# Kernel optimization log

Measured on AMD Instinct MI355X. Metric: run time of the kernel, lower is better.

## Reference

```python
import jax, jax.numpy as jnp
import numpy as np

R_MAX = 6.0
P = 6.0  # polynomial cutoff order


def poly_cutoff(r, r_max=R_MAX, p=P):
    # nequip PolynomialCutoff: smooth envelope, zero beyond r_max
    x = r / r_max
    out = (1.0
           - ((p + 1.0) * (p + 2.0) / 2.0) * x ** p
           + p * (p + 2.0) * x ** (p + 1.0)
           - (p * (p + 1.0) / 2.0) * x ** (p + 2.0))
    return out * (x < 1.0)


def setup_inputs() -> dict:
    key = jax.random.key(0)
    k1, k2, k3, k4 = jax.random.split(key, 4)
    N = 500000   # atoms
    E = 16000000  # edges
    T = 5        # species types
    edge_length = 0.5 + jax.random.uniform(k1, (E,), dtype=jnp.float32) * 5.5  # (0.5, 6.0)
    edge_index = jax.random.randint(k2, (2, E), 0, N, dtype=jnp.int64)
    species = jax.random.randint(k3, (N, 1), 0, T, dtype=jnp.int64)
    per_atom_energy = jax.random.normal(k4, (N, 1), dtype=jnp.float32)
    per_edge_scales = jnp.ones((T, T), dtype=jnp.float32)
    return {
        "edge_length": edge_length,
        "edge_index": edge_index,
        "species": species,
        "per_atom_energy": per_atom_energy,
        "per_edge_scales": per_edge_scales,
    }


def reference(edge_length, edge_index, species, per_atom_energy, per_edge_scales):
    N = species.shape[0]
    edge_center = edge_index[0]
    edge_neighbor = edge_index[1]
    sp = species[:, 0]                      # [N]
    center_sp = sp[edge_center]             # [E] gather
    neighbor_sp = sp[edge_neighbor]         # [E] gather
    l0 = per_edge_scales[center_sp, neighbor_sp]  # [E]
    # power-law repulsion with smooth cutoff
    edge_eng = (edge_length / l0) ** (-12.0) / 24.0 * l0 * poly_cutoff(edge_length)
    atom_eng = jax.ops.segment_sum(edge_eng, edge_center, num_segments=N)  # [N]
    return per_atom_energy + atom_eng[:, None]
```

## Files before the change

### kernel.cpp

```cpp
#include <hip/hip_runtime.h>
#include <stdint.h>

#define TPB_S  512
#define EPT    8
#define EPB    (TPB_S*EPT)
#define ABITS  10
#define APB    (1<<ABITS)
#define MAXB   512
#define NSH    8
#define TPB_A  1024
#define TPB_P  512
#define EDROP  1e-5f

__device__ __forceinline__ float fast_rcp(float r) {
#if defined(__has_builtin)
#if __has_builtin(__builtin_amdgcn_rcpf)
    float t = __builtin_amdgcn_rcpf(r);
    return t * fmaf(-r, t, 2.0f);
#else
    return 1.0f / r;
#endif
#else
    return 1.0f / r;
#endif
}

__device__ __forceinline__ float edge_energy_k(float r, float K) {
    float x = r * (1.0f / 6.0f);
    if (x >= 1.0f) return 0.0f;
    float x2 = x * x, x3 = x2 * x, x6 = x3 * x3;
    float cut = fmaf(x6, fmaf(x, fmaf(x, -21.0f, 48.0f), -28.0f), 1.0f);
    float t  = fast_rcp(r);
    float t2 = t * t, t4 = t2 * t2;
    float t12 = t4 * t4 * t4;
    return K * t12 * cut;
}
__device__ __forceinline__ float k_of_l0(float l0) {
    float l2 = l0 * l0, l4 = l2 * l2, l8 = l4 * l4;
    return l8 * l4 * l0 * (1.0f / 24.0f);
}

__device__ __forceinline__ uint32_t pack_rec(uint32_t c, float e) {
    e = fmaxf(e, 0.0f);
    uint32_t vb  = __float_as_uint(e);
    uint32_t v19 = (vb + 0x800u) >> 12;
    if (v19 > 0x7FFFFu) v19 = 0x7FFFFu;
    return ((c & (APB - 1u)) << 19) | v19;
}
__device__ __forceinline__ float unpack_val(uint32_t rec) {
    return __uint_as_float((rec & 0x7FFFFu) << 12);
}

__global__ __launch_bounds__(TPB_P) void k_prep(
    const float* __restrict__ scales, int tt,
    const float* __restrict__ pae, float* __restrict__ out, int N,
    uint32_t* __restrict__ cursors, uint32_t* __restrict__ uflag)
{
    int i = blockIdx.x * TPB_P + threadIdx.x;
    int i4 = i * 4;
    if (i4 + 4 <= N) {
        *(float4*)(out + i4) = *(const float4*)(pae + i4);
    } else if (i4 < N) {
        for (int j = i4; j < N; ++j) out[j] = pae[j];
    }
    if (i < MAXB * NSH) cursors[i] = 0u;
    if (blockIdx.x == 0 && threadIdx.x == 0) {
        float v0 = scales[0];
        bool same = true;
        for (int k = 1; k < tt; ++k) same &= (__float_as_uint(scales[k]) == __float_as_uint(v0));
        uflag[0] = same ? 1u : 0u;
        uflag[1] = __float_as_uint(v0);
        uflag[2] = __float_as_uint(k_of_l0(v0));
    }
}

__global__ __launch_bounds__(TPB_S) void k_scatter(
    const float* __restrict__ el, const int* __restrict__ ec,
    const int* __restrict__ en, const int* __restrict__ species,
    const float* __restrict__ scales, const uint32_t* __restrict__ uflag,
    uint32_t* __restrict__ cursors, uint32_t* __restrict__ bucketed,
    float* __restrict__ out, int E, int nb, int T, int cap)
{
    __shared__ uint32_t cs[EPB];
    __shared__ uint16_t bs[EPB];
    __shared__ uint32_t cnt[MAXB], lstart[MAXB], gbase[MAXB];
    __shared__ uint32_t wsum[8];

    for (int t = threadIdx.x; t < MAXB; t += TPB_S) cnt[t] = 0u;

    const uint32_t uni = uflag[0];
    const float    uK  = __uint_as_float(uflag[2]);
    const int shard = blockIdx.x & (NSH - 1);

    const int base = blockIdx.x * EPB;
    const int i0   = base + threadIdx.x * EPT;

    uint32_t recs[EPT]; int bkt[EPT]; uint32_t rnk[EPT];
#pragma unroll
    for (int j = 0; j < EPT; ++j) rnk[j] = 0xFFFFFFFFu;

    __syncthreads();

    if (i0 + EPT <= E) {
        float4 r0 = *(const float4*)(el + i0);
        float4 r1 = *(const float4*)(el + i0 + 4);
        int4   c0 = *(const int4*)(ec + i0);
        int4   c1 = *(const int4*)(ec + i0 + 4);
        float rr[EPT] = {r0.x,r0.y,r0.z,r0.w, r1.x,r1.y,r1.z,r1.w};
        int   cc[EPT] = {c0.x,c0.y,c0.z,c0.w, c1.x,c1.y,c1.z,c1.w};
        if (uni) {
#pragma unroll
            for (int j = 0; j < EPT; ++j) {
                float e = edge_energy_k(rr[j], uK);
                if (e >= EDROP) {
                    recs[j] = pack_rec((uint32_t)cc[j], e);
                    bkt[j]  = (int)((uint32_t)cc[j] >> ABITS);
                    rnk[j]  = atomicAdd(&cnt[bkt[j]], 1u);
                }
            }
        } else {
            int4 n0 = *(const int4*)(en + i0);
            int4 n1 = *(const int4*)(en + i0 + 4);
            int  nn[EPT] = {n0.x,n0.y,n0.z,n0.w, n1.x,n1.y,n1.z,n1.w};
#pragma unroll
            for (int j = 0; j < EPT; ++j) {
                float l0 = scales[species[cc[j]] * T + species[nn[j]]];
                float e = edge_energy_k(rr[j], k_of_l0(l0));
                if (e >= EDROP) {
                    recs[j] = pack_rec((uint32_t)cc[j], e);
                    bkt[j]  = (int)((uint32_t)cc[j] >> ABITS);
                    rnk[j]  = atomicAdd(&cnt[bkt[j]], 1u);
                }
            }
        }
    } else if (i0 < E) {
        int nval = E - i0;
#pragma unroll
        for (int j = 0; j < EPT; ++j) {
            if (j < nval) {
                int i = i0 + j;
                int c = ec[i];
                float K = uni ? uK
                              : k_of_l0(scales[species[c] * T + species[en[i]]]);
                float e = edge_energy_k(el[i], K);
                if (e >= EDROP) {
                    recs[j] = pack_rec((uint32_t)c, e);
                    bkt[j]  = (int)((uint32_t)c >> ABITS);
                    rnk[j]  = atomicAdd(&cnt[bkt[j]], 1u);
                }
            }
        }
    }
    __syncthreads();

    const int lane = threadIdx.x & 63;
    const int wv   = threadIdx.x >> 6;
    uint32_t v = (threadIdx.x < nb) ? cnt[threadIdx.x] : 0u;
    uint32_t incl = v;
#pragma unroll
    for (int d = 1; d < 64; d <<= 1) {
        uint32_t t = __shfl_up(incl, d);
        if (lane >= d) incl += t;
    }
    if (lane == 63) wsum[wv] = incl;
    __syncthreads();

    uint32_t g = 0;
    {
        uint32_t add = 0;
        for (int k = 0; k < wv; ++k) add += wsum[k];
        uint32_t excl = incl + add - v;
        if (threadIdx.x < nb) {
            lstart[threadIdx.x] = excl;
            if (v) g = atomicAdd(&cursors[shard * MAXB + threadIdx.x], v);
        }
    }
    __syncthreads();

#pragma unroll
    for (int j = 0; j < EPT; ++j) {
        if (rnk[j] != 0xFFFFFFFFu) {
            uint32_t r = lstart[bkt[j]] + rnk[j];
            cs[r] = recs[j];
            bs[r] = (uint16_t)bkt[j];
        }
    }
    if (threadIdx.x < nb) gbase[threadIdx.x] = g;
    __syncthreads();

    uint32_t tot = wsum[0] + wsum[1] + wsum[2] + wsum[3]
                 + wsum[4] + wsum[5] + wsum[6] + wsum[7];
    for (uint32_t k = threadIdx.x; k < tot; k += TPB_S) {
        int b = bs[k];
        uint32_t rec = cs[k];
        uint32_t pib = gbase[b] + (k - lstart[b]);
        if (pib < (uint32_t)cap) {
            bucketed[((size_t)b * NSH + shard) * (size_t)cap + pib] = rec;
        } else {
            int atom = (b << ABITS) | (int)(rec >> 19);
            atomicAdd(&out[atom], unpack_val(rec));
        }
    }
}

__global__ __launch_bounds__(TPB_A) void k_accum_out(
    const uint32_t* __restrict__ bucketed, const uint32_t* __restrict__ cursors,
    float* __restrict__ out, int N, int cap)
{
    __shared__ float acc[APB];
    const int b = blockIdx.x;
    acc[threadIdx.x] = 0.0f;
    __syncthreads();

    for (int s = 0; s < NSH; ++s) {
        uint32_t size = cursors[s * MAXB + b];
        if (size > (uint32_t)cap) size = (uint32_t)cap;
        const uint32_t* src = bucketed + ((size_t)b * NSH + s) * (size_t)cap;
        for (uint32_t k = (uint32_t)threadIdx.x * 4u; k < size; k += TPB_A * 4u) {
            if (k + 4u <= size) {
                uint4 r4 = *(const uint4*)(src + k);
                atomicAdd(&acc[r4.x >> 19], unpack_val(r4.x));
                atomicAdd(&acc[r4.y >> 19], unpack_val(r4.y));
                atomicAdd(&acc[r4.z >> 19], unpack_val(r4.z));
                atomicAdd(&acc[r4.w >> 19], unpack_val(r4.w));
            } else {
                for (uint32_t kk = k; kk < size; ++kk) {
                    uint32_t r = src[kk];
                    atomicAdd(&acc[r >> 19], unpack_val(r));
                }
            }
        }
    }
    __syncthreads();

    int g = (b << ABITS) + threadIdx.x;
    float a = acc[threadIdx.x];
    if (g < N && a != 0.0f) out[g] += a;
}

__global__ __launch_bounds__(256) void init_out_kernel(
    const float* __restrict__ pae, float* __restrict__ out, int N)
{
    int i = blockIdx.x * 256 + threadIdx.x;
    if (i < N) out[i] = pae[i];
}

__global__ __launch_bounds__(256) void edge_kernel_dev(
    const float* __restrict__ el, const int* __restrict__ ec,
    const int* __restrict__ en, const int* __restrict__ species,
    const float* __restrict__ scales, float* __restrict__ out, int E, int T)
{
    int i = blockIdx.x * 256 + threadIdx.x;
    if (i >= E) return;
    float r = el[i];
    int c = ec[i], n = en[i];
    float l0 = scales[species[c] * T + species[n]];
    float e = edge_energy_k(r, k_of_l0(l0));
    if (e >= EDROP) atomicAdd(&out[c], e);
}

extern "C" void kernel_launch(void* const* d_in, const int* in_sizes, int n_in,
                              void* d_out, int out_size, void* d_ws, size_t ws_size,
                              hipStream_t stream) {
    const float* el      = (const float*)d_in[0];
    const int*   eidx    = (const int*)  d_in[1];
    const int*   species = (const int*)  d_in[2];
    const float* pae     = (const float*)d_in[3];
    const float* scales  = (const float*)d_in[4];
    float*       out     = (float*)d_out;

    const int E = in_sizes[0];
    const int N = in_sizes[3];
    int T = 1;
    while (T * T < in_sizes[4]) ++T;

    const int nb  = (N + APB - 1) / APB;
    const int nb1 = (E + EPB - 1) / EPB;
    const int mean_s = E / (nb * NSH);
    const int cap = (int)(((size_t)mean_s * 9 / 8 + 1023) & ~(size_t)1023);

    size_t off = 0;
    auto take = [&](size_t bytes) { size_t o = off; off += (bytes + 15) & ~(size_t)15; return o; };
    size_t o_bucketed = take((size_t)nb * NSH * (size_t)cap * 4);
    size_t o_cursors  = take((size_t)MAXB * NSH * 4);
    size_t o_uflag    = take(16);
    const size_t need = off;

    if (nb <= MAXB && ws_size >= need) {
        char* ws = (char*)d_ws;
        uint32_t* bucketed = (uint32_t*)(ws + o_bucketed);
        uint32_t* cursors  = (uint32_t*)(ws + o_cursors);
        uint32_t* uflag    = (uint32_t*)(ws + o_uflag);

        int nthr = (N + 3) / 4;
        if (nthr < MAXB * NSH) nthr = MAXB * NSH;
        k_prep<<<(nthr + TPB_P - 1) / TPB_P, TPB_P, 0, stream>>>(
            scales, T * T, pae, out, N, cursors, uflag);
        k_scatter<<<nb1, TPB_S, 0, stream>>>(el, eidx, eidx + E, species, scales,
                                             uflag, cursors, bucketed, out,
                                             E, nb, T, cap);
        k_accum_out<<<nb, TPB_A, 0, stream>>>(bucketed, cursors, out, N, cap);
    } else {
        init_out_kernel<<<(N + 255) / 256, 256, 0, stream>>>(pae, out, N);
        edge_kernel_dev<<<(E + 255) / 256, 256, 0, stream>>>(
            el, eidx, eidx + E, species, scales, out, E, T);
    }
}
```

Baseline: 253.9 us.

## Scatter records directly to global buckets and precompute distance cutoff

Measured after the change: 256.9 us. Within noise of the previous version (+1.2%).

```diff
diff --git a/kernel.cpp b/kernel.cpp
--- a/kernel.cpp
+++ b/kernel.cpp
@@ -1,5 +1,6 @@
 #include <hip/hip_runtime.h>
 #include <stdint.h>
+#include <math.h>
 
 #define TPB_S  512
 #define EPT    8
@@ -68,9 +69,13 @@
         float v0 = scales[0];
         bool same = true;
         for (int k = 1; k < tt; ++k) same &= (__float_as_uint(scales[k]) == __float_as_uint(v0));
+        float K = k_of_l0(v0);
+        float rc = powf(K * (1.0f / EDROP), 1.0f / 12.0f);
+        if (!(rc < 6.0f)) rc = 6.0f;
         uflag[0] = same ? 1u : 0u;
         uflag[1] = __float_as_uint(v0);
-        uflag[2] = __float_as_uint(k_of_l0(v0));
+        uflag[2] = __float_as_uint(K);
+        uflag[3] = __float_as_uint(rc);
     }
 }
 
@@ -81,21 +86,19 @@
     uint32_t* __restrict__ cursors, uint32_t* __restrict__ bucketed,
     float* __restrict__ out, int E, int nb, int T, int cap)
 {
-    __shared__ uint32_t cs[EPB];
-    __shared__ uint16_t bs[EPB];
-    __shared__ uint32_t cnt[MAXB], lstart[MAXB], gbase[MAXB];
-    __shared__ uint32_t wsum[8];
-
-    for (int t = threadIdx.x; t < MAXB; t += TPB_S) cnt[t] = 0u;
-
-    const uint32_t uni = uflag[0];
-    const float    uK  = __uint_as_float(uflag[2]);
+    __shared__ uint32_t cnt[MAXB], gbase[MAXB];
+
+    cnt[threadIdx.x] = 0u;
+
+    const uint32_t uni  = uflag[0];
+    const float    uK   = __uint_as_float(uflag[2]);
+    const float    ucut = __uint_as_float(uflag[3]);
     const int shard = blockIdx.x & (NSH - 1);
 
     const int base = blockIdx.x * EPB;
     const int i0   = base + threadIdx.x * EPT;
 
-    uint32_t recs[EPT]; int bkt[EPT]; uint32_t rnk[EPT];
+    float rr[EPT]; uint32_t cc[EPT]; uint32_t rnk[EPT];
 #pragma unroll
     for (int j = 0; j < EPT; ++j) rnk[j] = 0xFFFFFFFFu;
 
@@ -106,17 +109,15 @@
         float4 r1 = *(const float4*)(el + i0 + 4);
         int4   c0 = *(const int4*)(ec + i0);
         int4   c1 = *(const int4*)(ec + i0 + 4);
-        float rr[EPT] = {r0.x,r0.y,r0.z,r0.w, r1.x,r1.y,r1.z,r1.w};
-        int   cc[EPT] = {c0.x,c0.y,c0.z,c0.w, c1.x,c1.y,c1.z,c1.w};
+        rr[0]=r0.x; rr[1]=r0.y; rr[2]=r0.z; rr[3]=r0.w;
+        rr[4]=r1.x; rr[5]=r1.y; rr[6]=r1.z; rr[7]=r1.w;
+        cc[0]=(uint32_t)c0.x; cc[1]=(uint32_t)c0.y; cc[2]=(uint32_t)c0.z; cc[3]=(uint32_t)c0.w;
+        cc[4]=(uint32_t)c1.x; cc[5]=(uint32_t)c1.y; cc[6]=(uint32_t)c1.z; cc[7]=(uint32_t)c1.w;
         if (uni) {
 #pragma unroll
             for (int j = 0; j < EPT; ++j) {
-                float e = edge_energy_k(rr[j], uK);
-                if (e >= EDROP) {
-                    recs[j] = pack_rec((uint32_t)cc[j], e);
-                    bkt[j]  = (int)((uint32_t)cc[j] >> ABITS);
-                    rnk[j]  = atomicAdd(&cnt[bkt[j]], 1u);
-                }
+                if (rr[j] <= ucut)
+                    rnk[j] = atomicAdd(&cnt[cc[j] >> ABITS], 1u);
             }
         } else {
             int4 n0 = *(const int4*)(en + i0);
@@ -127,9 +128,8 @@
                 float l0 = scales[species[cc[j]] * T + species[nn[j]]];
                 float e = edge_energy_k(rr[j], k_of_l0(l0));
                 if (e >= EDROP) {
-                    recs[j] = pack_rec((uint32_t)cc[j], e);
-                    bkt[j]  = (int)((uint32_t)cc[j] >> ABITS);
-                    rnk[j]  = atomicAdd(&cnt[bkt[j]], 1u);
+                    rr[j]  = e;
+                    rnk[j] = atomicAdd(&cnt[cc[j] >> ABITS], 1u);
                 }
             }
         }
@@ -139,66 +139,47 @@
         for (int j = 0; j < EPT; ++j) {
             if (j < nval) {
                 int i = i0 + j;
-                int c = ec[i];
-                float K = uni ? uK
-                              : k_of_l0(scales[species[c] * T + species[en[i]]]);
-                float e = edge_energy_k(el[i], K);
-                if (e >= EDROP) {
-                    recs[j] = pack_rec((uint32_t)c, e);
-                    bkt[j]  = (int)((uint32_t)c >> ABITS);
-                    rnk[j]  = atomicAdd(&cnt[bkt[j]], 1u);
+                cc[j] = (uint32_t)ec[i];
+                rr[j] = el[i];
+                if (uni) {
+                    if (rr[j] <= ucut)
+                        rnk[j] = atomicAdd(&cnt[cc[j] >> ABITS], 1u);
+                } else {
+                    float l0 = scales[species[cc[j]] * T + species[en[i]]];
+                    float e = edge_energy_k(rr[j], k_of_l0(l0));
+                    if (e >= EDROP) {
+                        rr[j]  = e;
+                        rnk[j] = atomicAdd(&cnt[cc[j] >> ABITS], 1u);
+                    }
                 }
             }
         }
     }
     __syncthreads();
 
-    const int lane = threadIdx.x & 63;
-    const int wv   = threadIdx.x >> 6;
-    uint32_t v = (threadIdx.x < nb) ? cnt[threadIdx.x] : 0u;
-    uint32_t incl = v;
-#pragma unroll
-    for (int d = 1; d < 64; d <<= 1) {
-        uint32_t t = __shfl_up(incl, d);
-        if (lane >= d) incl += t;
-    }
-    if (lane == 63) wsum[wv] = incl;
-    __syncthreads();
-
+    uint32_t v = cnt[threadIdx.x];
     uint32_t g = 0;
-    {
-        uint32_t add = 0;
-        for (int k = 0; k < wv; ++k) add += wsum[k];
-        uint32_t excl = incl + add - v;
-        if (threadIdx.x < nb) {
-            lstart[threadIdx.x] = excl;
-            if (v) g = atomicAdd(&cursors[shard * MAXB + threadIdx.x], v);
-        }
-    }
+    if (v) g = atomicAdd(&cursors[shard * MAXB + threadIdx.x], v);
+    if (uni) {
+#pragma unroll
+        for (int j = 0; j < EPT; ++j)
+            if (rnk[j] != 0xFFFFFFFFu) rr[j] = edge_energy_k(rr[j], uK);
+    }
+    gbase[threadIdx.x] = g;
     __syncthreads();
 
 #pragma unroll
     for (int j = 0; j < EPT; ++j) {
         if (rnk[j] != 0xFFFFFFFFu) {
-            uint32_t r = lstart[bkt[j]] + rnk[j];
-            cs[r] = recs[j];
-            bs[r] = (uint16_t)bkt[j];
-        }
-    }
-    if (threadIdx.x < nb) gbase[threadIdx.x] = g;
-    __syncthreads();
-
-    uint32_t tot = wsum[0] + wsum[1] + wsum[2] + wsum[3]
-                 + wsum[4] + wsum[5] + wsum[6] + wsum[7];
-    for (uint32_t k = threadIdx.x; k < tot; k += TPB_S) {
-        int b = bs[k];
-        uint32_t rec = cs[k];
-        uint32_t pib = gbase[b] + (k - lstart[b]);
-        if (pib < (uint32_t)cap) {
-            bucketed[((size_t)b * NSH + shard) * (size_t)cap + pib] = rec;
-        } else {
-            int atom = (b << ABITS) | (int)(rec >> 19);
-            atomicAdd(&out[atom], unpack_val(rec));
+            uint32_t b   = cc[j] >> ABITS;
+            uint32_t pib = gbase[b] + rnk[j];
+            uint32_t rec = pack_rec(cc[j], rr[j]);
+            if (pib < (uint32_t)cap) {
+                bucketed[((size_t)b * NSH + shard) * (size_t)cap + pib] = rec;
+            } else {
+                int atom = (int)((b << ABITS) | (rec >> 19));
+                atomicAdd(&out[atom], unpack_val(rec));
+            }
         }
     }
 }
@@ -212,22 +193,23 @@
     acc[threadIdx.x] = 0.0f;
     __syncthreads();
 
-    for (int s = 0; s < NSH; ++s) {
-        uint32_t size = cursors[s * MAXB + b];
-        if (size > (uint32_t)cap) size = (uint32_t)cap;
-        const uint32_t* src = bucketed + ((size_t)b * NSH + s) * (size_t)cap;
-        for (uint32_t k = (uint32_t)threadIdx.x * 4u; k < size; k += TPB_A * 4u) {
-            if (k + 4u <= size) {
-                uint4 r4 = *(const uint4*)(src + k);
-                atomicAdd(&acc[r4.x >> 19], unpack_val(r4.x));
-                atomicAdd(&acc[r4.y >> 19], unpack_val(r4.y));
-                atomicAdd(&acc[r4.z >> 19], unpack_val(r4.z));
-                atomicAdd(&acc[r4.w >> 19], unpack_val(r4.w));
-            } else {
-                for (uint32_t kk = k; kk < size; ++kk) {
-                    uint32_t r = src[kk];
-                    atomicAdd(&acc[r >> 19], unpack_val(r));
-                }
+    const int s = threadIdx.x >> 7;
+    const int t = threadIdx.x & 127;
+    uint32_t size = cursors[s * MAXB + b];
+    if (size > (uint32_t)cap) size = (uint32_t)cap;
+    const uint32_t* src = bucketed + ((size_t)b * NSH + s) * (size_t)cap;
+
+    for (uint32_t k = (uint32_t)t * 4u; k < size; k += 128u * 4u) {
+        if (k + 4u <= size) {
+            uint4 r4 = *(const uint4*)(src + k);
+            atomicAdd(&acc[r4.x >> 19], unpack_val(r4.x));
+            atomicAdd(&acc[r4.y >> 19], unpack_val(r4.y));
+            atomicAdd(&acc[r4.z >> 19], unpack_val(r4.z));
+            atomicAdd(&acc[r4.w >> 19], unpack_val(r4.w));
+        } else {
+            for (uint32_t kk = k; kk < size; ++kk) {
+                uint32_t r = src[kk];
+                atomicAdd(&acc[r >> 19], unpack_val(r));
             }
         }
     }
```
